# Kernel tuning notes

Hardware: AMD Instinct MI355X
Metric: run time of the kernel (lower is better)

The kernel has to match this reference:

```python
import jax, jax.numpy as jnp
import numpy as np

NUM_EMBEDDINGS = 8192
EMBEDDING_DIM = 256
COMMITMENT_COST = 0.25
DECAY = 0.99
EPS = 1e-05


def setup_inputs() -> dict:
    key = jax.random.key(0)
    k1, k2, k3 = jax.random.split(key, 3)
    x = jax.random.normal(k1, (16, 256, 32, 32), dtype=jnp.float32)
    emb = jax.random.normal(k2, (NUM_EMBEDDINGS, EMBEDDING_DIM), dtype=jnp.float32) * 0.1
    emb = emb / jnp.linalg.norm(emb, axis=1, keepdims=True)  # F.normalize(dim=1)
    return {
        "x": x,
        "embedding": emb,
        "cluster_size": jnp.ones((NUM_EMBEDDINGS,), dtype=jnp.float32),
        "embed_avg": emb,
    }


def reference(x, embedding, cluster_size, embed_avg):
    K, D = embedding.shape
    n = x.ndim
    # permute channels (dim 1) to last, flatten to [N, D]
    perm_fwd = (0,) + tuple(range(2, n)) + (1,)
    px = jnp.transpose(x, perm_fwd)
    flat = px.reshape(-1, D)  # [N, D]

    # squared L2 distances (monotone in cdist p=2) -> argmin nearest code
    d = (
        jnp.sum(flat * flat, axis=1, keepdims=True)
        - 2.0 * (flat @ embedding.T)
        + jnp.sum(embedding * embedding, axis=1)
    )  # [N, K]
    idx = jnp.argmin(d, axis=1)  # [N]

    # gather-by-index instead of one-hot @ embedding (same math)
    quantized = embedding[idx].reshape(px.shape)
    perm_back = (0, n - 1) + tuple(range(1, n - 1))
    quantized = jnp.transpose(quantized, perm_back)  # back to x layout

    # EMA buffer updates (training path, no_grad in torch)
    counts = jax.ops.segment_sum(
        jnp.ones_like(idx, dtype=flat.dtype), idx, num_segments=K
    )  # == encodings.sum(0)
    new_cluster_size = cluster_size * DECAY + (1.0 - DECAY) * counts
    dw = jax.ops.segment_sum(flat, idx, num_segments=K)  # == encodings.T @ flat
    new_embed_avg = embed_avg * DECAY + (1.0 - DECAY) * dw
    new_embedding = new_embed_avg / jnp.maximum(new_cluster_size, EPS)[:, None]

    # commitment loss (quantized detached)
    loss = COMMITMENT_COST * jnp.mean((x - jax.lax.stop_gradient(quantized)) ** 2)

    # straight-through estimator
    quantized_st = x + jax.lax.stop_gradient(quantized - x)

    avg_probs = counts / flat.shape[0]  # == encodings.mean(0)
    perplexity = jnp.exp(-jnp.sum(avg_probs * jnp.log(avg_probs + 1e-10)))

    return (quantized_st, loss, perplexity, new_embedding, new_cluster_size, new_embed_avg)
```

## Files before the change

### kernel.cpp

```cpp
#include <hip/hip_runtime.h>
#include <stdint.h>

#define K_CODES 8192
#define D 256
#define NROWS 16384
#define NELEM 4194304

#define WS_ENORM   0x00000u
#define WS_KEYS    0x08000u
#define WS_ICOUNTS 0x28000u
#define WS_CURSOR  0x30000u
#define WS_BASE    0x38000u
#define WS_ROWLIST 0x40000u
#define WS_PART    0x50000u
#define WS_XHI     0x60000u
#define WS_XLO     (WS_XHI + 0x800000u)
#define WS_EHI     (WS_XLO + 0x800000u)
#define WS_ELO     (WS_EHI + 0x400000u)

#define O_QST  0
#define O_LOSS 4194304
#define O_PERP 4194305
#define O_EMB  4194306
#define O_CS   6291458
#define O_EAVG 6299650

typedef unsigned short u16;
typedef __attribute__((ext_vector_type(8))) short bf16x8;
typedef __attribute__((ext_vector_type(4))) float f32x4;

__device__ __forceinline__ u16 f2bf(float f) {
    uint32_t u = __float_as_uint(f);
    u += 0x7FFFu + ((u >> 16) & 1u);
    return (u16)(u >> 16);
}
__device__ __forceinline__ float bf2f(u16 h) {
    return __uint_as_float(((uint32_t)h) << 16);
}

__device__ __forceinline__ void glds16(const u16* g, u16* lds_base) {
    __builtin_amdgcn_global_load_lds(
        (const __attribute__((address_space(1))) uint32_t*)g,
        (__attribute__((address_space(3))) uint32_t*)lds_base, 16, 0, 0);
}

__global__ __launch_bounds__(256) void prep_emb_kernel(const float* __restrict__ emb,
                                                       u16* __restrict__ eh,
                                                       u16* __restrict__ el,
                                                       float* __restrict__ enorm) {
    const int k = blockIdx.x, t = threadIdx.x;
    const size_t i = (size_t)k * D + t;
    const float v = emb[i];
    const u16 h = f2bf(v);
    const float r = v - bf2f(h);
    eh[i] = h;
    el[i] = f2bf(r);
    float s = v * v;
#pragma unroll
    for (int off = 32; off; off >>= 1) s += __shfl_down(s, off, 64);
    __shared__ float sm[4];
    if ((t & 63) == 0) sm[t >> 6] = s;
    __syncthreads();
    if (t == 0) enorm[k] = sm[0] + sm[1] + sm[2] + sm[3];
}

__global__ __launch_bounds__(256) void prep_x_kernel(const float* __restrict__ x,
                                                     u16* __restrict__ xhi,
                                                     u16* __restrict__ xlo) {
    __shared__ u16 Lh[64][72];
    __shared__ u16 Ll[64][72];
    const int hw0 = blockIdx.x << 6;
    const int c0 = blockIdx.y << 6;
    const int b = blockIdx.z;
    const int t = threadIdx.x, l = t & 63, w = t >> 6;
#pragma unroll
    for (int i = 0; i < 16; ++i) {
        const int cl = w * 16 + i;
        const float v = x[(((size_t)(b * 256 + c0 + cl)) << 10) + hw0 + l];
        const u16 h = f2bf(v);
        Lh[l][cl] = h;
        Ll[l][cl] = f2bf(v - bf2f(h));
    }
    __syncthreads();
    const int r = t >> 2, cs = t & 3;
    const size_t n = (((size_t)b) << 10) + hw0 + r;
    const size_t o = n * D + c0 + cs * 16;
    *(uint4*)&xhi[o]     = *(const uint4*)&Lh[r][cs * 16];
    *(uint4*)&xhi[o + 8] = *(const uint4*)&Lh[r][cs * 16 + 8];
    *(uint4*)&xlo[o]     = *(const uint4*)&Ll[r][cs * 16];
    *(uint4*)&xlo[o + 8] = *(const uint4*)&Ll[r][cs * 16 + 8];
}

#define BM 128
#define BN 128
#define SLICES 2
#define CT_PER 32

__global__ __launch_bounds__(256, 1) void dist_kernel(const u16* __restrict__ xhi,
                                                      const u16* __restrict__ xlo,
                                                      const u16* __restrict__ ehi,
                                                      const u16* __restrict__ elo,
                                                      const float* __restrict__ enorm,
                                                      unsigned long long* __restrict__ keys) {
    extern __shared__ __align__(16) u16 lds[];

    const int tid = threadIdx.x;
    const int l = tid & 63, w = tid >> 6;
    const int wr = w >> 1, wc = w & 1;
    const int slice = blockIdx.x;
    const int n0 = blockIdx.y * BM;
    const int md = l & 15, quad = l >> 4;

#pragma unroll
    for (int wd = 0; wd < 16; ++wd) {
        const int win = w * 16 + wd;
        const int rA = 2 * win + (l >> 5);
        const int g = (l & 31) ^ (rA & 31);
        const size_t src = (size_t)(n0 + rA) * D + g * 8;
        glds16(xhi + src, &lds[win * 512]);
        glds16(xlo + src, &lds[32768 + win * 512]);
    }

    const int rloc = l >> 3, sB = l & 7, gB = sB ^ rloc;
    const u16* PB[4];
#pragma unroll
    for (int w8 = 0; w8 < 4; ++w8) {
        const u16* pl = (gB & 4) ? elo : ehi;
        PB[w8] = pl + (size_t)(slice * 4096 + w * 32 + w8 * 8 + rloc) * D + (gB & 3) * 8;
    }
    const int bdst = 65536 + (w * 32) * 64;

#pragma unroll
    for (int w8 = 0; w8 < 4; ++w8) glds16(PB[w8], &lds[bdst + w8 * 512]);

    int rbase[4], rh[4];
#pragma unroll
    for (int i = 0; i < 4; ++i) {
        const int rA = wr * 64 + i * 16 + md;
        rbase[i] = rA * 256;
        rh[i] = rA & 31;
    }
    int offBH[4], offBL[4];
#pragma unroll
    for (int j = 0; j < 4; ++j) {
        const int cr = wc * 64 + j * 16 + md;
        offBH[j] = 65536 + cr * 64 + ((quad) ^ (md & 7)) * 8;
        offBL[j] = 65536 + cr * 64 + ((quad + 4) ^ (md & 7)) * 8;
    }

    float rbv[4][4];
    int rbi[4][4];
#pragma unroll
    for (int i = 0; i < 4; ++i)
#pragma unroll
        for (int r = 0; r < 4; ++r) { rbv[i][r] = 1e30f; rbi[i][r] = 0; }

    f32x4 acc[4][4];
#pragma unroll
    for (int i = 0; i < 4; ++i)
#pragma unroll
        for (int j = 0; j < 4; ++j) acc[i][j] = (f32x4)0.f;

    bf16x8 fah[2][4], fal[2][4], fbh[2][4], fbl[2][4];

    float ecr[4];
#pragma unroll
    for (int j = 0; j < 4; ++j) ecr[j] = enorm[slice * 4096 + wc * 64 + j * 16 + md];

    for (int ct = 0; ct < CT_PER; ++ct) {
#pragma unroll
        for (int kt = 0; kt < 8; ++kt) {
            __syncthreads();
            if (kt < 7) {
                const int soff = ct * 32768 + (kt + 1) * 32;
                const int db = bdst + (((kt + 1) & 1) << 13);
#pragma unroll
                for (int w8 = 0; w8 < 4; ++w8) glds16(PB[w8] + soff, &lds[db + w8 * 512]);
            } else if (ct < CT_PER - 1) {
                const int soff = (ct + 1) * 32768;
#pragma unroll
                for (int w8 = 0; w8 < 4; ++w8) glds16(PB[w8] + soff, &lds[bdst + w8 * 512]);
            }
            const int p = kt & 1, bufo = p << 13;
#pragma unroll
            for (int i = 0; i < 4; ++i) {
                const int slot = ((kt << 2) | quad) ^ rh[i];
                fah[p][i] = *(const bf16x8*)&lds[rbase[i] + slot * 8];
                fal[p][i] = *(const bf16x8*)&lds[32768 + rbase[i] + slot * 8];
            }
#pragma unroll
            for (int j = 0; j < 4; ++j) {
                fbh[p][j] = *(const bf16x8*)&lds[bufo + offBH[j]];
                fbl[p][j] = *(const bf16x8*)&lds[bufo + offBL[j]];
            }
            if (kt > 0 || ct > 0) {
                const int q = p ^ 1;
#pragma unroll
                for (int i = 0; i < 4; ++i)
#pragma unroll
                    for (int j = 0; j < 4; ++j) {
                        acc[i][j] = __builtin_amdgcn_mfma_f32_16x16x32_bf16(fah[q][i], fbh[q][j], acc[i][j], 0, 0, 0);
                        acc[i][j] = __builtin_amdgcn_mfma_f32_16x16x32_bf16(fah[q][i], fbl[q][j], acc[i][j], 0, 0, 0);
                        acc[i][j] = __builtin_amdgcn_mfma_f32_16x16x32_bf16(fal[q][i], fbh[q][j], acc[i][j], 0, 0, 0);
                    }
                if (kt == 0) {
                    const int gc0 = slice * 4096 + (ct - 1) * 128;
#pragma unroll
                    for (int i = 0; i < 4; ++i)
#pragma unroll
                        for (int r = 0; r < 4; ++r)
#pragma unroll
                            for (int j = 0; j < 4; ++j) {
                                const float s = fmaf(-2.f, acc[i][j][r], ecr[j]);
                                const int ci = gc0 + wc * 64 + j * 16 + md;
                                if (s < rbv[i][r]) { rbv[i][r] = s; rbi[i][r] = ci; }
                            }
#pragma unroll
                    for (int j = 0; j < 4; ++j)
                        ecr[j] = enorm[slice * 4096 + ct * 128 + wc * 64 + j * 16 + md];
#pragma unroll
                    for (int i = 0; i < 4; ++i)
#pragma unroll
                        for (int j = 0; j < 4; ++j) acc[i][j] = (f32x4)0.f;
                }
            }
        }
    }

    {
#pragma unroll
        for (int i = 0; i < 4; ++i)
#pragma unroll
            for (int j = 0; j < 4; ++j) {
                acc[i][j] = __builtin_amdgcn_mfma_f32_16x16x32_bf16(fah[1][i], fbh[1][j], acc[i][j], 0, 0, 0);
                acc[i][j] = __builtin_amdgcn_mfma_f32_16x16x32_bf16(fah[1][i], fbl[1][j], acc[i][j], 0, 0, 0);
                acc[i][j] = __builtin_amdgcn_mfma_f32_16x16x32_bf16(fal[1][i], fbh[1][j], acc[i][j], 0, 0, 0);
            }
        const int gc0 = slice * 4096 + (CT_PER - 1) * 128;
#pragma unroll
        for (int i = 0; i < 4; ++i)
#pragma unroll
            for (int r = 0; r < 4; ++r)
#pragma unroll
                for (int j = 0; j < 4; ++j) {
                    const float s = fmaf(-2.f, acc[i][j][r], ecr[j]);
                    const int ci = gc0 + wc * 64 + j * 16 + md;
                    if (s < rbv[i][r]) { rbv[i][r] = s; rbi[i][r] = ci; }
                }
    }

#pragma unroll
    for (int i = 0; i < 4; ++i)
#pragma unroll
        for (int r = 0; r < 4; ++r) {
            float bv = rbv[i][r];
            int bi = rbi[i][r];
#pragma unroll
            for (int m = 1; m < 16; m <<= 1) {
                const float ov = __shfl_xor(bv, m, 64);
                const int oi = __shfl_xor(bi, m, 64);
                if (ov < bv || (ov == bv && oi < bi)) { bv = ov; bi = oi; }
            }
            if (md == 0) {
                unsigned int u = __float_as_uint(bv);
                u = (u & 0x80000000u) ? ~u : (u | 0x80000000u);
                const unsigned long long key = ((unsigned long long)u << 32) | (unsigned int)bi;
                atomicMin(&keys[n0 + wr * 64 + i * 16 + quad * 4 + r], key);
            }
        }
}

__global__ __launch_bounds__(256) void quant_loss_kernel(const float* __restrict__ x,
                                                         const float* __restrict__ emb,
                                                         const unsigned long long* __restrict__ keys,
                                                         float* __restrict__ out,
                                                         float* __restrict__ partials,
                                                         int* __restrict__ icounts) {
    const int blk = blockIdx.x;
    const int b = blk >> 4;
    const int hw0 = (blk & 15) << 6;
    const int l = threadIdx.x & 63;
    const int cq = threadIdx.x >> 6;
    const int hw = hw0 + l;
    const int n = (b << 10) + hw;
    const int code = (int)(keys[n] & 0xFFFFFFFFull);
    if (threadIdx.x < 64) atomicAdd(&icounts[code], 1);
    const float* erow = emb + (size_t)code * D;
    const float* xb = x + (((size_t)b * 256) << 10) + hw;
    float* ob = out + O_QST + (((size_t)b * 256) << 10) + hw;
    float lsum = 0.f;
#pragma unroll 4
    for (int c = cq; c < D; c += 4) {
        const float xv = xb[(size_t)c << 10];
        const float ev = erow[c];
        ob[(size_t)c << 10] = xv + (ev - xv);
        const float d = xv - ev;
        lsum = fmaf(d, d, lsum);
    }
    __shared__ float sm[4];
    const int lane = threadIdx.x & 63, wv = threadIdx.x >> 6;
#pragma unroll
    for (int off = 32; off; off >>= 1) lsum += __shfl_down(lsum, off, 64);
    if (lane == 0) sm[wv] = lsum;
    __syncthreads();
    if (threadIdx.x == 0) partials[blockIdx.x] = sm[0] + sm[1] + sm[2] + sm[3];
}

__global__ __launch_bounds__(256) void scan_final_kernel(const int* __restrict__ icounts,
                                                         int* __restrict__ basearr,
                                                         const float* __restrict__ partials,
                                                         float* __restrict__ out) {
    const int t = threadIdx.x, lane = t & 63, w = t >> 6;
    int loc = 0;
    float ps = 0.f;
    for (int i = 0; i < 32; ++i) {
        const int c = icounts[t * 32 + i];
        loc += c;
        const float p = (float)c * (1.0f / 16384.0f);
        ps += p * logf(p + 1e-10f);
    }
    int v = loc;
#pragma unroll
    for (int off = 1; off < 64; off <<= 1) {
        const int u = __shfl_up(v, off, 64);
        if (lane >= off) v += u;
    }
    __shared__ int wsum[4];
    __shared__ float fs[8];
    if (lane == 63) wsum[w] = v;
    float lp = partials[t];
#pragma unroll
    for (int off = 32; off; off >>= 1) {
        lp += __shfl_down(lp, off, 64);
        ps += __shfl_down(ps, off, 64);
    }
    if (lane == 0) { fs[w] = lp; fs[4 + w] = ps; }
    __syncthreads();
    int pre = 0;
    for (int i = 0; i < w; ++i) pre += wsum[i];
    int b = pre + v - loc;
    for (int i = 0; i < 32; ++i) {
        basearr[t * 32 + i] = b;
        b += icounts[t * 32 + i];
    }
    if (t == 0) {
        out[O_LOSS] = 0.25f * ((fs[0] + fs[1] + fs[2] + fs[3]) / 4194304.0f);
        out[O_PERP] = expf(-(fs[4] + fs[5] + fs[6] + fs[7]));
    }
}

__global__ __launch_bounds__(256) void slot_kernel(const unsigned long long* __restrict__ keys,
                                                   const int* __restrict__ basearr,
                                                   int* __restrict__ cursor,
                                                   int* __restrict__ rowlist) {
    const int n = blockIdx.x * 256 + threadIdx.x;
    const int code = (int)(keys[n] & 0xFFFFFFFFull);
    const int pos = atomicAdd(&cursor[code], 1);
    rowlist[basearr[code] + pos] = n;
}

__global__ __launch_bounds__(256) void gather_ema_kernel(const u16* __restrict__ xhi,
                                                         const u16* __restrict__ xlo,
                                                         const int* __restrict__ icounts,
                                                         const int* __restrict__ basearr,
                                                         const int* __restrict__ rowlist,
                                                         const float* __restrict__ embed_avg,
                                                         const float* __restrict__ cluster_size,
                                                         float* __restrict__ out) {
    const int k = blockIdx.x, c = threadIdx.x;
    const int cnt = icounts[k], b0 = basearr[k];
    float s = 0.f;
    for (int t = 0; t < cnt; ++t) {
        const int n = rowlist[b0 + t];
        s += bf2f(xhi[(size_t)n * D + c]) + bf2f(xlo[(size_t)n * D + c]);
    }
    const float ncs = cluster_size[k] * 0.99f + 0.01f * (float)cnt;
    const size_t i = (size_t)k * D + c;
    const float na = embed_avg[i] * 0.99f + 0.01f * s;
    out[O_EAVG + i] = na;
    out[O_EMB + i] = na / fmaxf(ncs, 1e-5f);
    if (c == 0) out[O_CS + k] = ncs;
}

extern "C" void kernel_launch(void* const* d_in, const int* in_sizes, int n_in,
                              void* d_out, int out_size, void* d_ws, size_t ws_size,
                              hipStream_t stream) {
    const float* x            = (const float*)d_in[0];
    const float* emb          = (const float*)d_in[1];
    const float* cluster_size = (const float*)d_in[2];
    const float* embed_avg    = (const float*)d_in[3];
    float* out = (float*)d_out;
    char* ws = (char*)d_ws;

    float* enorm = (float*)(ws + WS_ENORM);
    unsigned long long* keys = (unsigned long long*)(ws + WS_KEYS);
    int* icounts = (int*)(ws + WS_ICOUNTS);
    int* cursor = (int*)(ws + WS_CURSOR);
    int* basearr = (int*)(ws + WS_BASE);
    int* rowlist = (int*)(ws + WS_ROWLIST);
    float* partials = (float*)(ws + WS_PART);
    u16* xhi = (u16*)(ws + WS_XHI);
    u16* xlo = (u16*)(ws + WS_XLO);
    u16* ehi = (u16*)(ws + WS_EHI);
    u16* elo = (u16*)(ws + WS_ELO);

    static int lds_attr_set = 0;
    if (!lds_attr_set) {
        hipFuncSetAttribute((const void*)dist_kernel,
                            hipFuncAttributeMaxDynamicSharedMemorySize, 163840);
        lds_attr_set = 1;
    }

    hipMemsetAsync(ws + WS_ICOUNTS, 0, 0x10000, stream);
    hipMemsetAsync(ws + WS_KEYS, 0xFF, NROWS * 8, stream);

    prep_emb_kernel<<<K_CODES, 256, 0, stream>>>(emb, ehi, elo, enorm);
    prep_x_kernel<<<dim3(16, 4, 16), 256, 0, stream>>>(x, xhi, xlo);
    dist_kernel<<<dim3(SLICES, NROWS / BM), 256, 163840, stream>>>(xhi, xlo, ehi, elo, enorm, keys);
    quant_loss_kernel<<<256, 256, 0, stream>>>(x, emb, keys, out, partials, icounts);
    scan_final_kernel<<<1, 256, 0, stream>>>(icounts, basearr, partials, out);
    slot_kernel<<<NROWS / 256, 256, 0, stream>>>(keys, basearr, cursor, rowlist);
    gather_ema_kernel<<<K_CODES, 256, 0, stream>>>(xhi, xlo, icounts, basearr, rowlist,
                                                   embed_avg, cluster_size, out);
}
```

Before: 301.6 us.

## Fuse prep kernels and memsets; keep x-lo fragments in registers with per-wave B staging

Merges the embedding prep, x prep and the two memsets into one launch to cut launch overhead. In the distance kernel, the low-part A fragments are loaded once into registers, which frees LDS so each wave can stage its own B tiles. The per-k-step __syncthreads is replaced by a waitcnt plus sched_barrier, with a prefetch across the tile boundary. This raises register pressure, and each wave pair now redundantly loads B columns, adding global traffic.

```diff
diff --git a/kernel.cpp b/kernel.cpp
--- a/kernel.cpp
+++ b/kernel.cpp
@@ -44,51 +44,60 @@
         (__attribute__((address_space(3))) uint32_t*)lds_base, 16, 0, 0);
 }
 
-__global__ __launch_bounds__(256) void prep_emb_kernel(const float* __restrict__ emb,
-                                                       u16* __restrict__ eh,
-                                                       u16* __restrict__ el,
-                                                       float* __restrict__ enorm) {
-    const int k = blockIdx.x, t = threadIdx.x;
-    const size_t i = (size_t)k * D + t;
-    const float v = emb[i];
-    const u16 h = f2bf(v);
-    const float r = v - bf2f(h);
-    eh[i] = h;
-    el[i] = f2bf(r);
-    float s = v * v;
-#pragma unroll
-    for (int off = 32; off; off >>= 1) s += __shfl_down(s, off, 64);
-    __shared__ float sm[4];
-    if ((t & 63) == 0) sm[t >> 6] = s;
-    __syncthreads();
-    if (t == 0) enorm[k] = sm[0] + sm[1] + sm[2] + sm[3];
-}
-
-__global__ __launch_bounds__(256) void prep_x_kernel(const float* __restrict__ x,
-                                                     u16* __restrict__ xhi,
-                                                     u16* __restrict__ xlo) {
+__global__ __launch_bounds__(256) void prep_kernel(const float* __restrict__ emb,
+                                                   const float* __restrict__ x,
+                                                   u16* __restrict__ eh,
+                                                   u16* __restrict__ el,
+                                                   float* __restrict__ enorm,
+                                                   u16* __restrict__ xhi,
+                                                   u16* __restrict__ xlo,
+                                                   unsigned long long* __restrict__ keys,
+                                                   int* __restrict__ icounts,
+                                                   int* __restrict__ cursor) {
     __shared__ u16 Lh[64][72];
     __shared__ u16 Ll[64][72];
-    const int hw0 = blockIdx.x << 6;
-    const int c0 = blockIdx.y << 6;
-    const int b = blockIdx.z;
-    const int t = threadIdx.x, l = t & 63, w = t >> 6;
-#pragma unroll
-    for (int i = 0; i < 16; ++i) {
-        const int cl = w * 16 + i;
-        const float v = x[(((size_t)(b * 256 + c0 + cl)) << 10) + hw0 + l];
+    const int bid = blockIdx.x, t = threadIdx.x;
+    if (bid < 8192) {
+        const int k = bid;
+        const size_t i = (size_t)k * D + t;
+        const float v = emb[i];
         const u16 h = f2bf(v);
-        Lh[l][cl] = h;
-        Ll[l][cl] = f2bf(v - bf2f(h));
-    }
-    __syncthreads();
-    const int r = t >> 2, cs = t & 3;
-    const size_t n = (((size_t)b) << 10) + hw0 + r;
-    const size_t o = n * D + c0 + cs * 16;
-    *(uint4*)&xhi[o]     = *(const uint4*)&Lh[r][cs * 16];
-    *(uint4*)&xhi[o + 8] = *(const uint4*)&Lh[r][cs * 16 + 8];
-    *(uint4*)&xlo[o]     = *(const uint4*)&Ll[r][cs * 16];
-    *(uint4*)&xlo[o + 8] = *(const uint4*)&Ll[r][cs * 16 + 8];
+        eh[i] = h;
+        el[i] = f2bf(v - bf2f(h));
+        float s = v * v;
+#pragma unroll
+        for (int off = 32; off; off >>= 1) s += __shfl_down(s, off, 64);
+        __shared__ float sm[4];
+        if ((t & 63) == 0) sm[t >> 6] = s;
+        __syncthreads();
+        if (t == 0) enorm[k] = sm[0] + sm[1] + sm[2] + sm[3];
+    } else if (bid < 9216) {
+        const int px = bid - 8192;
+        const int hw0 = (px & 15) << 6;
+        const int c0 = ((px >> 4) & 3) << 6;
+        const int b = px >> 6;
+        const int l = t & 63, w = t >> 6;
+#pragma unroll
+        for (int i = 0; i < 16; ++i) {
+            const int cl = w * 16 + i;
+            const float v = x[(((size_t)(b * 256 + c0 + cl)) << 10) + hw0 + l];
+            const u16 h = f2bf(v);
+            Lh[l][cl] = h;
+            Ll[l][cl] = f2bf(v - bf2f(h));
+        }
+        __syncthreads();
+        const int r = t >> 2, cs = t & 3;
+        const size_t n = (((size_t)b) << 10) + hw0 + r;
+        const size_t o = n * D + c0 + cs * 16;
+        *(uint4*)&xhi[o]     = *(const uint4*)&Lh[r][cs * 16];
+        *(uint4*)&xhi[o + 8] = *(const uint4*)&Lh[r][cs * 16 + 8];
+        *(uint4*)&xlo[o]     = *(const uint4*)&Ll[r][cs * 16];
+        *(uint4*)&xlo[o + 8] = *(const uint4*)&Ll[r][cs * 16 + 8];
+    } else {
+        const int n = (bid - 9216) * 256 + t;
+        keys[n] = ~0ull;
+        if (n < K_CODES) { icounts[n] = 0; cursor[n] = 0; }
+    }
 }
 
 #define BM 128
@@ -121,18 +130,6 @@
         glds16(xlo + src, &lds[32768 + win * 512]);
     }
 
-    const int rloc = l >> 3, sB = l & 7, gB = sB ^ rloc;
-    const u16* PB[4];
-#pragma unroll
-    for (int w8 = 0; w8 < 4; ++w8) {
-        const u16* pl = (gB & 4) ? elo : ehi;
-        PB[w8] = pl + (size_t)(slice * 4096 + w * 32 + w8 * 8 + rloc) * D + (gB & 3) * 8;
-    }
-    const int bdst = 65536 + (w * 32) * 64;
-
-#pragma unroll
-    for (int w8 = 0; w8 < 4; ++w8) glds16(PB[w8], &lds[bdst + w8 * 512]);
-
     int rbase[4], rh[4];
 #pragma unroll
     for (int i = 0; i < 4; ++i) {
@@ -140,12 +137,37 @@
         rbase[i] = rA * 256;
         rh[i] = rA & 31;
     }
+
+    __syncthreads();
+
+    bf16x8 falo[8][4];
+#pragma unroll
+    for (int kt = 0; kt < 8; ++kt)
+#pragma unroll
+        for (int i = 0; i < 4; ++i) {
+            const int slot = ((kt << 2) | quad) ^ rh[i];
+            falo[kt][i] = *(const bf16x8*)&lds[32768 + rbase[i] + slot * 8];
+        }
+
+    __syncthreads();
+
+    const int WB = 32768 + w * 8192;
+    const int rloc = l >> 3, sB = l & 7, gB = sB ^ rloc;
+    const u16* PB[8];
+#pragma unroll
+    for (int c8 = 0; c8 < 8; ++c8) {
+        const u16* pl = (gB & 4) ? elo : ehi;
+        PB[c8] = pl + (size_t)(slice * 4096 + wc * 64 + c8 * 8 + rloc) * D + (gB & 3) * 8;
+    }
+#pragma unroll
+    for (int c8 = 0; c8 < 8; ++c8) glds16(PB[c8], &lds[WB + c8 * 512]);
+
     int offBH[4], offBL[4];
 #pragma unroll
     for (int j = 0; j < 4; ++j) {
-        const int cr = wc * 64 + j * 16 + md;
-        offBH[j] = 65536 + cr * 64 + ((quad) ^ (md & 7)) * 8;
-        offBL[j] = 65536 + cr * 64 + ((quad + 4) ^ (md & 7)) * 8;
+        const int cloc = j * 16 + md;
+        offBH[j] = WB + cloc * 64 + ((quad) ^ (md & 7)) * 8;
+        offBL[j] = WB + cloc * 64 + ((quad + 4) ^ (md & 7)) * 8;
     }
 
     float rbv[4][4];
@@ -161,7 +183,7 @@
 #pragma unroll
         for (int j = 0; j < 4; ++j) acc[i][j] = (f32x4)0.f;
 
-    bf16x8 fah[2][4], fal[2][4], fbh[2][4], fbl[2][4];
+    bf16x8 fahi[2][4], fbh[2][4], fbl[2][4];
 
     float ecr[4];
 #pragma unroll
@@ -170,23 +192,21 @@
     for (int ct = 0; ct < CT_PER; ++ct) {
 #pragma unroll
         for (int kt = 0; kt < 8; ++kt) {
-            __syncthreads();
-            if (kt < 7) {
-                const int soff = ct * 32768 + (kt + 1) * 32;
-                const int db = bdst + (((kt + 1) & 1) << 13);
-#pragma unroll
-                for (int w8 = 0; w8 < 4; ++w8) glds16(PB[w8] + soff, &lds[db + w8 * 512]);
-            } else if (ct < CT_PER - 1) {
-                const int soff = (ct + 1) * 32768;
-#pragma unroll
-                for (int w8 = 0; w8 < 4; ++w8) glds16(PB[w8] + soff, &lds[bdst + w8 * 512]);
-            }
-            const int p = kt & 1, bufo = p << 13;
+            __builtin_amdgcn_s_waitcnt(0x0F70);
+            __builtin_amdgcn_sched_barrier(0);
+            const int m = ct * 8 + kt;
+            if (m < CT_PER * 8 - 1) {
+                const int m1 = m + 1;
+                const int soff = (m1 >> 3) * 32768 + (m1 & 7) * 32;
+                const int db = WB + ((m1 & 1) << 12);
+#pragma unroll
+                for (int c8 = 0; c8 < 8; ++c8) glds16(PB[c8] + soff, &lds[db + c8 * 512]);
+            }
+            const int p = kt & 1, bufo = p << 12;
 #pragma unroll
             for (int i = 0; i < 4; ++i) {
                 const int slot = ((kt << 2) | quad) ^ rh[i];
-                fah[p][i] = *(const bf16x8*)&lds[rbase[i] + slot * 8];
-                fal[p][i] = *(const bf16x8*)&lds[32768 + rbase[i] + slot * 8];
+                fahi[p][i] = *(const bf16x8*)&lds[rbase[i] + slot * 8];
             }
 #pragma unroll
             for (int j = 0; j < 4; ++j) {
@@ -195,13 +215,14 @@
             }
             if (kt > 0 || ct > 0) {
                 const int q = p ^ 1;
+                const int kq = (kt + 7) & 7;
 #pragma unroll
                 for (int i = 0; i < 4; ++i)
 #pragma unroll
                     for (int j = 0; j < 4; ++j) {
-                        acc[i][j] = __builtin_amdgcn_mfma_f32_16x16x32_bf16(fah[q][i], fbh[q][j], acc[i][j], 0, 0, 0);
-                        acc[i][j] = __builtin_amdgcn_mfma_f32_16x16x32_bf16(fah[q][i], fbl[q][j], acc[i][j], 0, 0, 0);
-                        acc[i][j] = __builtin_amdgcn_mfma_f32_16x16x32_bf16(fal[q][i], fbh[q][j], acc[i][j], 0, 0, 0);
+                        acc[i][j] = __builtin_amdgcn_mfma_f32_16x16x32_bf16(fahi[q][i], fbh[q][j], acc[i][j], 0, 0, 0);
+                        acc[i][j] = __builtin_amdgcn_mfma_f32_16x16x32_bf16(fahi[q][i], fbl[q][j], acc[i][j], 0, 0, 0);
+                        acc[i][j] = __builtin_amdgcn_mfma_f32_16x16x32_bf16(falo[kq][i], fbh[q][j], acc[i][j], 0, 0, 0);
                     }
                 if (kt == 0) {
                     const int gc0 = slice * 4096 + (ct - 1) * 128;
@@ -232,9 +253,9 @@
         for (int i = 0; i < 4; ++i)
 #pragma unroll
             for (int j = 0; j < 4; ++j) {
-                acc[i][j] = __builtin_amdgcn_mfma_f32_16x16x32_bf16(fah[1][i], fbh[1][j], acc[i][j], 0, 0, 0);
-                acc[i][j] = __builtin_amdgcn_mfma_f32_16x16x32_bf16(fah[1][i], fbl[1][j], acc[i][j], 0, 0, 0);
-                acc[i][j] = __builtin_amdgcn_mfma_f32_16x16x32_bf16(fal[1][i], fbh[1][j], acc[i][j], 0, 0, 0);
+                acc[i][j] = __builtin_amdgcn_mfma_f32_16x16x32_bf16(fahi[1][i], fbh[1][j], acc[i][j], 0, 0, 0);
+                acc[i][j] = __builtin_amdgcn_mfma_f32_16x16x32_bf16(fahi[1][i], fbl[1][j], acc[i][j], 0, 0, 0);
+                acc[i][j] = __builtin_amdgcn_mfma_f32_16x16x32_bf16(falo[7][i], fbh[1][j], acc[i][j], 0, 0, 0);
             }
         const int gc0 = slice * 4096 + (CT_PER - 1) * 128;
 #pragma unroll
@@ -407,16 +428,13 @@
     static int lds_attr_set = 0;
     if (!lds_attr_set) {
         hipFuncSetAttribute((const void*)dist_kernel,
-                            hipFuncAttributeMaxDynamicSharedMemorySize, 163840);
+                            hipFuncAttributeMaxDynamicSharedMemorySize, 131072);
         lds_attr_set = 1;
     }
 
-    hipMemsetAsync(ws + WS_ICOUNTS, 0, 0x10000, stream);
-    hipMemsetAsync(ws + WS_KEYS, 0xFF, NROWS * 8, stream);
-
-    prep_emb_kernel<<<K_CODES, 256, 0, stream>>>(emb, ehi, elo, enorm);
-    prep_x_kernel<<<dim3(16, 4, 16), 256, 0, stream>>>(x, xhi, xlo);
-    dist_kernel<<<dim3(SLICES, NROWS / BM), 256, 163840, stream>>>(xhi, xlo, ehi, elo, enorm, keys);
+    prep_kernel<<<9280, 256, 0, stream>>>(emb, x, ehi, elo, enorm, xhi, xlo,
+                                          keys, icounts, cursor);
+    dist_kernel<<<dim3(SLICES, NROWS / BM), 256, 131072, stream>>>(xhi, xlo, ehi, elo, enorm, keys);
     quant_loss_kernel<<<256, 256, 0, stream>>>(x, emb, keys, out, partials, icounts);
     scan_final_kernel<<<1, 256, 0, stream>>>(icounts, basearr, partials, out);
     slot_kernel<<<NROWS / 256, 256, 0, stream>>>(keys, basearr, cursor, rowlist);
```

New measurement: 293.6 us. 2.7% less time.
